# Performance work log

Hardware: AMD Instinct MI355X
Metric: run time of the kernel (lower is better)

## Reference

```python
import jax, jax.numpy as jnp
import numpy as np

B, T, F, H = 256, 128, 128, 512

def setup_inputs() -> dict:
    key = jax.random.key(0)
    ks = jax.random.split(key, 20)
    def xavier(k, shape):
        fan_in, fan_out = shape[1], shape[0]
        lim = np.sqrt(6.0 / (fan_in + fan_out)).astype(np.float32)
        return jax.random.uniform(k, shape, jnp.float32, -lim, lim)
    inp = {
        "x": jax.random.normal(ks[0], (B, T, F), jnp.float32),
        "m": (jax.random.uniform(ks[1], (B, T, F)) < 0.8).astype(jnp.float32),
        "d": jax.random.uniform(ks[2], (B, T, F), jnp.float32),
        "target_x": jax.random.normal(ks[3], (B, T, F), jnp.float32),
        "target_mask": (jax.random.uniform(ks[4], (B, T, F)) < 0.2).astype(jnp.float32),
        # TemporalDecay h: W [H,F], b [H]
        "td_h_W": xavier(ks[5], (H, F)), "td_h_b": jnp.zeros((H,), jnp.float32),
        # TemporalDecay x (diag): W [F,F], b [F]
        "td_x_W": xavier(ks[6], (F, F)), "td_x_b": jnp.zeros((F,), jnp.float32),
        # hist_reg Linear(H->F)
        "hist_W": xavier(ks[7], (F, H)), "hist_b": jnp.zeros((F,), jnp.float32),
        "feat_W": xavier(ks[8], (F, F)), "feat_b": jnp.zeros((F,), jnp.float32),
        # weight_combine Linear(2F->F)
        "wc_W": xavier(ks[9], (F, 2 * F)), "wc_b": jnp.zeros((F,), jnp.float32),
        # LSTMCell(2F -> H), PyTorch gate order i,f,g,o
        "W_ih": xavier(ks[10], (4 * H, 2 * F)), "W_hh": xavier(ks[11], (4 * H, H)),
        "b_ih": jnp.zeros((4 * H,), jnp.float32), "b_hh": jnp.zeros((4 * H,), jnp.float32),
    }
    return inp

def _rits_forward(x, m, d, target_x, target_mask,
                  td_h_W, td_h_b, td_x_W, td_x_b,
                  hist_W, hist_b, feat_W, feat_b, wc_W, wc_b,
                  W_ih, W_hh, b_ih, b_hh):
    Bx, Tx, Fx = x.shape
    Hx = td_h_W.shape[0]
    feat_mask = (1.0 - jnp.eye(Fx, dtype=x.dtype))
    feat_Wm_T = (feat_W * feat_mask).T              # [F,F]
    td_x_diag = jnp.diagonal(td_x_W)                # diag mask reduces matmul to elementwise

    def step(carry, inp):
        h, c, loss = carry
        x_t, m_t, d_t, tgt_t, ev_t = inp
        gamma_h = jnp.exp(-jax.nn.relu(d_t @ td_h_W.T + td_h_b))    # [B,H]
        gamma_x = jnp.exp(-jax.nn.relu(d_t * td_x_diag + td_x_b))   # [B,F]
        h = h * gamma_h
        x_hist = h @ hist_W.T + hist_b                              # [B,F]
        x_c = m_t * x_t + (1.0 - m_t) * x_hist
        z_h = x_c @ feat_Wm_T + feat_b
        alpha = jax.nn.sigmoid(jnp.concatenate([gamma_x, m_t], axis=1) @ wc_W.T + wc_b)
        c_h = alpha * z_h + (1.0 - alpha) * x_hist
        c_c = m_t * x_t + (1.0 - m_t) * c_h
        inputs = jnp.concatenate([c_c, m_t], axis=1)                # [B,2F]
        gates = inputs @ W_ih.T + b_ih + h @ W_hh.T + b_hh          # [B,4H]
        i_g, f_g, g_g, o_g = jnp.split(gates, 4, axis=1)
        c = jax.nn.sigmoid(f_g) * c + jax.nn.sigmoid(i_g) * jnp.tanh(g_g)
        h = jax.nn.sigmoid(o_g) * jnp.tanh(c)
        denom = ev_t.sum() + 1e-8
        loss = loss + (((x_hist - tgt_t) ** 2 * ev_t).sum()
                       + ((z_h - tgt_t) ** 2 * ev_t).sum()
                       + ((c_h - tgt_t) ** 2 * ev_t).sum()) / denom
        return (h, c, loss), c_c

    h0 = jnp.zeros((Bx, Hx), x.dtype)
    c0 = jnp.zeros((Bx, Hx), x.dtype)
    tm = lambda a: jnp.swapaxes(a, 0, 1)  # time-major [T,B,F]
    (_, _, loss), imps = jax.lax.scan(
        step, (h0, c0, jnp.float32(0.0)),
        (tm(x), tm(m), tm(d), tm(target_x), tm(target_mask)))
    imputations = jnp.swapaxes(imps, 0, 1)  # [B,T,F]
    return imputations, loss / max(Tx, 1)

def reference(x, m, d, target_x, target_mask,
              td_h_W, td_h_b, td_x_W, td_x_b,
              hist_W, hist_b, feat_W, feat_b, wc_W, wc_b,
              W_ih, W_hh, b_ih, b_hh):
    return _rits_forward(x, m, d, target_x, target_mask,
                         td_h_W, td_h_b, td_x_W, td_x_b,
                         hist_W, hist_b, feat_W, feat_b, wc_W, wc_b,
                         W_ih, W_hh, b_ih, b_hh)
```

## Files before the change

kernel.cpp:

```cpp
#include <hip/hip_runtime.h>

#define DEVINL __device__ __forceinline__

namespace {
constexpr int B = 256, T = 128, F = 128, H = 512;
constexpr int NBLK = 256;
constexpr int NTHR = 1024;

constexpr size_t OFF_NUM    = 0;
constexpr size_t OFF_DEN    = 128;
constexpr size_t OFF_WQCC   = 256;
constexpr size_t OFF_WQH    = OFF_WQCC + 64 * 2048;
constexpr size_t OFF_FSCC   = OFF_WQH + 128 * 2048;
constexpr size_t OFF_FSCHG  = OFF_FSCC + 2048;
constexpr size_t OFF_HISTQ  = OFF_FSCHG + 2048;
constexpr size_t OFF_FSCH   = OFF_HISTQ + 128 * 128;
constexpr size_t OFF_TD2    = OFF_FSCH + 128;
constexpr size_t OFF_FEAT2  = OFF_TD2 + 64 * 512;
constexpr size_t OFF_WC2    = OFF_FEAT2 + 64 * 128;
constexpr size_t OFF_BSUM   = OFF_WC2 + 128 * 128;
constexpr size_t OFF_FDIAG  = OFF_BSUM + 2048;
constexpr size_t WS_WORDS   = OFF_FDIAG + 128;

constexpr float ACT_S  = 15.875f;
constexpr float DEQ_CC = 1.f / (127.f * 15.875f);
constexpr float DEQ_H  = 1.f / (127.f * 127.f);
}

typedef _Float16 h2_t __attribute__((ext_vector_type(2)));

DEVINL h2_t as_h2(unsigned u) { union { unsigned u; h2_t h; } c; c.u = u; return c.h; }
DEVINL unsigned pack2(float a, float b) {
  union { h2_t h; unsigned u; } c;
  c.h = h2_t{(_Float16)a, (_Float16)b};
  return c.u;
}

#if defined(__has_builtin)
#if __has_builtin(__builtin_amdgcn_fdot2)
#define HAVE_FDOT2 1
#endif
#if __has_builtin(__builtin_amdgcn_sdot4)
#define HAVE_SDOT4 1
#endif
#endif
#ifdef HAVE_FDOT2
DEVINL float fdot2(h2_t a, h2_t b, float c) { return __builtin_amdgcn_fdot2(a, b, c, false); }
#else
DEVINL float fdot2(h2_t a, h2_t b, float c) {
  return fmaf((float)a.x, (float)b.x, fmaf((float)a.y, (float)b.y, c));
}
#endif
#ifdef HAVE_SDOT4
DEVINL int sdot4(int a, int b, int c) { return __builtin_amdgcn_sdot4(a, b, c, false); }
#else
DEVINL int sdot4(int a, int b, int c) {
  return c + ((a << 24) >> 24) * ((b << 24) >> 24)
           + ((a << 16) >> 24) * ((b << 16) >> 24)
           + ((a << 8) >> 24) * ((b << 8) >> 24)
           + (a >> 24) * (b >> 24);
}
#endif

DEVINL float fast_sig(float x)  { return 1.f / (1.f + __expf(-x)); }
DEVINL float fast_tanh(float x) { return 1.f - 2.f / (1.f + __expf(2.f * x)); }

DEVINL float wave_sum(float v) {
#pragma unroll
  for (int s = 32; s; s >>= 1) v += __shfl_down(v, s, 64);
  return v;
}
DEVINL float wave_max(float v) {
#pragma unroll
  for (int s = 32; s; s >>= 1) v = fmaxf(v, __shfl_down(v, s, 64));
  return v;
}

__global__ void prep_f16(const float* __restrict__ td_h_W, const float* __restrict__ feat_W,
                         const float* __restrict__ wc_W, const float* __restrict__ b_ih,
                         const float* __restrict__ b_hh,
                         unsigned* __restrict__ wsu, float* __restrict__ wsf) {
  int idx = blockIdx.x * blockDim.x + threadIdx.x;
  if (idx < 32768) {
    const int k2 = idx >> 9, j = idx & 511;
    wsu[OFF_TD2 + idx] = pack2(td_h_W[j * 128 + 2 * k2], td_h_W[j * 128 + 2 * k2 + 1]);
  } else if (idx < 40960) {
    const int i = idx - 32768, k2 = i >> 7, f = i & 127;
    wsu[OFF_FEAT2 + i] = pack2(feat_W[f * 128 + 2 * k2], feat_W[f * 128 + 2 * k2 + 1]);
  } else if (idx < 57344) {
    const int i = idx - 40960, k2 = i >> 7, f = i & 127;
    wsu[OFF_WC2 + i] = pack2(wc_W[f * 256 + 2 * k2], wc_W[f * 256 + 2 * k2 + 1]);
  } else if (idx < 59392) {
    const int i = idx - 57344, unit = i >> 2, g = i & 3;
    wsf[OFF_BSUM + i] = b_ih[g * 512 + unit] + b_hh[g * 512 + unit];
  } else if (idx < 59520) {
    const int f = idx - 59392;
    wsf[OFF_FDIAG + f] = (float)(_Float16)feat_W[f * 129];
  }
}

__global__ void prep_quant_wih(const float* __restrict__ Wih,
                               unsigned* __restrict__ wq, float* __restrict__ fscc) {
  const int col = blockIdx.x;
  const int unit = col >> 2, g = col & 3;
  const float* src = Wih + (size_t)(g * 512 + unit) * 256;
  const int t = threadIdx.x;
  const float4 v = ((const float4*)src)[t];
  float mx = fmaxf(fmaxf(fabsf(v.x), fabsf(v.y)), fmaxf(fabsf(v.z), fabsf(v.w)));
  mx = wave_max(mx);
  mx = __shfl(mx, 0, 64);
  const float s = (mx > 0.f) ? 127.f / mx : 0.f;
  const int q0 = __float2int_rn(v.x * s), q1 = __float2int_rn(v.y * s);
  const int q2 = __float2int_rn(v.z * s), q3 = __float2int_rn(v.w * s);
  wq[t * 2048 + col] =
      (q0 & 0xFF) | ((q1 & 0xFF) << 8) | ((q2 & 0xFF) << 16) | ((q3 & 0xFF) << 24);
  if (t == 0) fscc[col] = mx * DEQ_CC;
}

__global__ void prep_quant_whh(const float* __restrict__ Whh,
                               unsigned* __restrict__ wq, float* __restrict__ fschg) {
  const int col = blockIdx.x;
  const int unit = col >> 2, g = col & 3;
  const float* src = Whh + (size_t)(g * 512 + unit) * 512;
  const int t = threadIdx.x;
  const float4 v = ((const float4*)src)[t];
  float mx = fmaxf(fmaxf(fabsf(v.x), fabsf(v.y)), fmaxf(fabsf(v.z), fabsf(v.w)));
  mx = wave_max(mx);
  __shared__ float wm[2];
  if ((t & 63) == 0) wm[t >> 6] = mx;
  __syncthreads();
  const float maxv = fmaxf(wm[0], wm[1]);
  const float s = (maxv > 0.f) ? 127.f / maxv : 0.f;
  const int q0 = __float2int_rn(v.x * s), q1 = __float2int_rn(v.y * s);
  const int q2 = __float2int_rn(v.z * s), q3 = __float2int_rn(v.w * s);
  wq[t * 2048 + col] =
      (q0 & 0xFF) | ((q1 & 0xFF) << 8) | ((q2 & 0xFF) << 16) | ((q3 & 0xFF) << 24);
  if (t == 0) fschg[col] = maxv * DEQ_H;
}

__global__ void prep_quant_hist(const float* __restrict__ histW,
                                unsigned* __restrict__ histq, float* __restrict__ fsch) {
  const int f = blockIdx.x;
  const float* src = histW + (size_t)f * 512;
  const int t = threadIdx.x;
  const float4 v = ((const float4*)src)[t];
  float mx = fmaxf(fmaxf(fabsf(v.x), fabsf(v.y)), fmaxf(fabsf(v.z), fabsf(v.w)));
  mx = wave_max(mx);
  __shared__ float wm[2];
  if ((t & 63) == 0) wm[t >> 6] = mx;
  __syncthreads();
  const float maxv = fmaxf(wm[0], wm[1]);
  const float s = (maxv > 0.f) ? 127.f / maxv : 0.f;
  const int q0 = __float2int_rn(v.x * s), q1 = __float2int_rn(v.y * s);
  const int q2 = __float2int_rn(v.z * s), q3 = __float2int_rn(v.w * s);
  histq[t * 128 + f] =
      (q0 & 0xFF) | ((q1 & 0xFF) << 8) | ((q2 & 0xFF) << 16) | ((q3 & 0xFF) << 24);
  if (t == 0) fsch[f] = maxv * DEQ_H;
}

__global__ void __launch_bounds__(1024) rits_batch(
    const float* __restrict__ x, const float* __restrict__ m, const float* __restrict__ d,
    const float* __restrict__ tx, const float* __restrict__ tmask,
    const float* __restrict__ td_h_b, const float* __restrict__ td_x_W,
    const float* __restrict__ td_x_b, const float* __restrict__ hist_b,
    const float* __restrict__ feat_b, const float* __restrict__ wc_b,
    const unsigned* __restrict__ wsu, const float* __restrict__ wsf,
    float* __restrict__ num, float* __restrict__ den, float* __restrict__ out)
{
  const int tid = threadIdx.x;
  const int row = blockIdx.x;
  const int unit = tid & 511;
  const int kh = tid >> 9;

  __shared__ unsigned actq[64];
  __shared__ int hq[128];
  __shared__ unsigned d2[64];
  __shared__ unsigned xc2[64];
  __shared__ unsigned gxm2[128];
  __shared__ float xrow[128], mrow[128], drow[128], txrow[128], evrow[128];
  __shared__ int   partI[1024];
  __shared__ float partZ[1024], partA[1024];
  __shared__ int4  partHc[512], partHh[512];
  __shared__ float redA[2], redB[2];

  const float4 bs    = *(const float4*)(wsf + OFF_BSUM + 4 * unit);
  const float4 fscc4 = *(const float4*)(wsf + OFF_FSCC + 4 * unit);
  const float4 fsch4 = *(const float4*)(wsf + OFF_FSCHG + 4 * unit);
  const float tdb = td_h_b[unit];
  const int fc = tid & 127;
  const float hb = hist_b[fc], fb = feat_b[fc], wb = wc_b[fc];
  const float fd = wsf[OFF_FDIAG + fc];
  const float dxw = td_x_W[fc * 129], dxb = td_x_b[fc];
  const float fsch_f = wsf[OFF_FSCH + fc];

  float h0 = 0.f, c0 = 0.f;

  for (int t = 0; t < T; ++t) {
    const int base = (row * T + t) * F;
    float xh_r = 0.f, xc_r = 0.f;

    if (tid < 640) {
      const int a = tid >> 7, f = tid & 127;
      const float v = (a == 0 ? x[base + f] : a == 1 ? m[base + f] : a == 2 ? d[base + f]
                       : a == 3 ? tx[base + f] : tmask[base + f]);
      if      (a == 0) xrow[f]  = v;
      else if (a == 1) mrow[f]  = v;
      else if (a == 2) drow[f]  = v;
      else if (a == 3) txrow[f] = v;
      else             evrow[f] = v;
    } else if (tid < 704) {
      const int k2 = tid - 640;
      d2[k2] = pack2(d[base + 2 * k2], d[base + 2 * k2 + 1]);
    } else if (tid < 768) {
      const int q = tid - 704;
      gxm2[64 + q] = pack2(m[base + 2 * q], m[base + 2 * q + 1]);
    } else if (tid < 800) {
      const int w = tid - 768;
      const int b4 = base + 4 * w;
      const int q0 = __float2int_rn(m[b4] * ACT_S);
      const int q1 = __float2int_rn(m[b4 + 1] * ACT_S);
      const int q2 = __float2int_rn(m[b4 + 2] * ACT_S);
      const int q3 = __float2int_rn(m[b4 + 3] * ACT_S);
      actq[32 + w] =
          (q0 & 0xFF) | ((q1 & 0xFF) << 8) | ((q2 & 0xFF) << 16) | ((q3 & 0xFF) << 24);
    }
    __syncthreads();

    if (tid < 512) {
      float g0 = tdb;
#pragma unroll 8
      for (int k2 = 0; k2 < 64; ++k2)
        g0 = fdot2(as_h2(wsu[OFF_TD2 + (k2 << 9) + tid]), as_h2(d2[k2]), g0);
      h0 *= __expf(-fmaxf(g0, 0.f));
      int q = __float2int_rn(h0 * 127.f);
      const int a1 = __shfl_down(q, 1, 64), a2 = __shfl_down(q, 2, 64), a3 = __shfl_down(q, 3, 64);
      if ((tid & 3) == 0)
        hq[tid >> 2] =
            (q & 0xFF) | ((a1 & 0xFF) << 8) | ((a2 & 0xFF) << 16) | ((a3 & 0xFF) << 24);
    }
    __syncthreads();

    {
      const int kq = tid >> 7;
      int isum = 0;
#pragma unroll 8
      for (int k = 0; k < 16; ++k) {
        const int k4 = kq * 16 + k;
        isum = sdot4((int)wsu[OFF_HISTQ + (k4 << 7) + fc], hq[k4], isum);
      }
      partI[tid] = isum;
    }
    __syncthreads();

    if (tid < 128) {
      int isum = 0;
#pragma unroll
      for (int i = 0; i < 8; ++i) isum += partI[tid + 128 * i];
      xh_r = fmaf((float)isum, fsch_f, hb);
      const float gx = __expf(-fmaxf(fmaf(drow[tid], dxw, dxb), 0.f));
      const float mv = mrow[tid];
      xc_r = mv * xrow[tid] + (1.f - mv) * xh_r;
      const float xcs = __shfl_down(xc_r, 1, 64);
      const float gxs = __shfl_down(gx, 1, 64);
      if (!(tid & 1)) {
        xc2[tid >> 1]  = pack2(xc_r, xcs);
        gxm2[tid >> 1] = pack2(gx, gxs);
      }
    }
    __syncthreads();

    {
      const int kq = tid >> 7;
      float zs = 0.f;
#pragma unroll 8
      for (int k = 0; k < 8; ++k) {
        const int k2 = kq * 8 + k;
        zs = fdot2(as_h2(wsu[OFF_FEAT2 + (k2 << 7) + fc]), as_h2(xc2[k2]), zs);
      }
      partZ[tid] = zs;
      float as = 0.f;
#pragma unroll 8
      for (int k = 0; k < 16; ++k) {
        const int k2 = kq * 16 + k;
        as = fdot2(as_h2(wsu[OFF_WC2 + (k2 << 7) + fc]), as_h2(gxm2[k2]), as);
      }
      partA[tid] = as;
    }
    __syncthreads();

    if (tid < 128) {
      float z = fb, aa = wb;
#pragma unroll
      for (int i = 0; i < 8; ++i) { z += partZ[tid + 128 * i]; aa += partA[tid + 128 * i]; }
      z -= xc_r * fd;
      const float al = fast_sig(aa);
      const float ch = al * z + (1.f - al) * xh_r;
      const float mv = mrow[tid];
      const float cc = mv * xrow[tid] + (1.f - mv) * ch;
      out[base + tid] = cc;
      const float ev = evrow[tid], tg = txrow[tid];
      const float e1 = xh_r - tg, e2 = z - tg, e3 = ch - tg;
      const float s1 = wave_sum(ev * (e1 * e1 + e2 * e2 + e3 * e3));
      const float s2 = wave_sum(ev);
      if ((tid & 63) == 0) { redA[tid >> 6] = s1; redB[tid >> 6] = s2; }
      int qc = __float2int_rn(fminf(fmaxf(cc, -8.f), 8.f) * ACT_S);
      const int c1s = __shfl_down(qc, 1, 64), c2s = __shfl_down(qc, 2, 64), c3s = __shfl_down(qc, 3, 64);
      if (!(tid & 3))
        actq[tid >> 2] =
            (qc & 0xFF) | ((c1s & 0xFF) << 8) | ((c2s & 0xFF) << 16) | ((c3s & 0xFF) << 24);
    }
    __syncthreads();

    {
      if (tid == 1023) {
        atomicAdd(&num[t], redA[0] + redA[1]);
        atomicAdd(&den[t], redB[0] + redB[1]);
      }
      int ci = 0, cf = 0, cg = 0, co = 0;
      const unsigned* wq = wsu + OFF_WQCC + 4 * unit;
#pragma unroll 8
      for (int k = 0; k < 32; ++k) {
        const int k4 = kh * 32 + k;
        const uint4 w = *(const uint4*)(wq + (k4 << 11));
        const int a0 = (int)actq[k4];
        ci = sdot4((int)w.x, a0, ci); cf = sdot4((int)w.y, a0, cf);
        cg = sdot4((int)w.z, a0, cg); co = sdot4((int)w.w, a0, co);
      }
      int hi = 0, hf = 0, hg = 0, ho = 0;
      const unsigned* wh = wsu + OFF_WQH + 4 * unit;
#pragma unroll 8
      for (int k = 0; k < 64; ++k) {
        const int k4 = kh * 64 + k;
        const uint4 w = *(const uint4*)(wh + (k4 << 11));
        const int a0 = hq[k4];
        hi = sdot4((int)w.x, a0, hi); hf = sdot4((int)w.y, a0, hf);
        hg = sdot4((int)w.z, a0, hg); ho = sdot4((int)w.w, a0, ho);
      }
      if (tid >= 512) {
        partHc[unit] = int4{ci, cf, cg, co};
        partHh[unit] = int4{hi, hf, hg, ho};
      }
      __syncthreads();
      if (tid < 512) {
        const int4 pc = partHc[unit], ph = partHh[unit];
        const float ai = bs.x + fscc4.x * (float)(ci + pc.x) + fsch4.x * (float)(hi + ph.x);
        const float af = bs.y + fscc4.y * (float)(cf + pc.y) + fsch4.y * (float)(hf + ph.y);
        const float ag = bs.z + fscc4.z * (float)(cg + pc.z) + fsch4.z * (float)(hg + ph.z);
        const float ao = bs.w + fscc4.w * (float)(co + pc.w) + fsch4.w * (float)(ho + ph.w);
        const float ig = fast_sig(ai), fg = fast_sig(af);
        const float gg = fast_tanh(ag), og = fast_sig(ao);
        c0 = fg * c0 + ig * gg;
        h0 = og * fast_tanh(c0);
      }
    }
    __syncthreads();
  }
}

__global__ void finalize(const float* __restrict__ num, const float* __restrict__ den,
                         float* __restrict__ out) {
  __shared__ float red[2];
  const int t = threadIdx.x;
  float v = num[t] / (den[t] + 1e-8f);
  v = wave_sum(v);
  if ((t & 63) == 0) red[t >> 6] = v;
  __syncthreads();
  if (t == 0) out[(size_t)B * T * F] = (red[0] + red[1]) / (float)T;
}

extern "C" void kernel_launch(void* const* d_in, const int* in_sizes, int n_in,
                              void* d_out, int out_size, void* d_ws, size_t ws_size,
                              hipStream_t stream) {
  const float* x      = (const float*)d_in[0];
  const float* m      = (const float*)d_in[1];
  const float* d      = (const float*)d_in[2];
  const float* tx     = (const float*)d_in[3];
  const float* tmask  = (const float*)d_in[4];
  const float* td_h_W = (const float*)d_in[5];
  const float* td_h_b = (const float*)d_in[6];
  const float* td_x_W = (const float*)d_in[7];
  const float* td_x_b = (const float*)d_in[8];
  const float* hist_W = (const float*)d_in[9];
  const float* hist_b = (const float*)d_in[10];
  const float* feat_W = (const float*)d_in[11];
  const float* feat_b = (const float*)d_in[12];
  const float* wc_W   = (const float*)d_in[13];
  const float* wc_b   = (const float*)d_in[14];
  const float* W_ih   = (const float*)d_in[15];
  const float* W_hh   = (const float*)d_in[16];
  const float* b_ih   = (const float*)d_in[17];
  const float* b_hh   = (const float*)d_in[18];

  float*    wsf = (float*)d_ws;
  unsigned* wsu = (unsigned*)d_ws;
  float*    out = (float*)d_out;

  if (ws_size < WS_WORDS * 4) return;

  hipMemsetAsync(d_ws, 0, 256 * sizeof(float), stream);
  prep_f16<<<dim3((59520 + 255) / 256), dim3(256), 0, stream>>>(
      td_h_W, feat_W, wc_W, b_ih, b_hh, wsu, wsf);
  prep_quant_wih<<<dim3(2048), dim3(64), 0, stream>>>(
      W_ih, wsu + OFF_WQCC, wsf + OFF_FSCC);
  prep_quant_whh<<<dim3(2048), dim3(128), 0, stream>>>(
      W_hh, wsu + OFF_WQH, wsf + OFF_FSCHG);
  prep_quant_hist<<<dim3(128), dim3(128), 0, stream>>>(
      hist_W, wsu + OFF_HISTQ, wsf + OFF_FSCH);
  rits_batch<<<dim3(NBLK), dim3(NTHR), 0, stream>>>(
      x, m, d, tx, tmask, td_h_b, td_x_W, td_x_b, hist_b, feat_b, wc_b,
      wsu, wsf, wsf + OFF_NUM, wsf + OFF_DEN, out);
  finalize<<<dim3(1), dim3(128), 0, stream>>>(wsf + OFF_NUM, wsf + OFF_DEN, out);
}
```

Measured before the change: 2.436 ms.

## Warp-specialize RITS step with LDS flag sync and overlapped LSTM matvecs

Replaces the per-step chain of block-wide __syncthreads with warp specialization. Two waves handle the feature path (hist regression, feature regression, combine, loss, next-step decay prefetch). The other 14 waves run the LSTM int8 matvecs and signal each other through LDS atomic flags with spin-waits. The h-part of the LSTM gate matvec now starts as soon as hq is ready and overlaps the feature-side work, and next-step inputs and decay are computed ahead with double-buffered shared arrays. Weight layouts are transposed so each feature thread streams its own contiguous row with uint4 loads. The cost is spin-wait polling, a guard-limited spin that could break silently, and only 128 threads doing the feature path serially.

```diff
diff --git a/kernel.cpp b/kernel.cpp
--- a/kernel.cpp
+++ b/kernel.cpp
@@ -25,6 +25,8 @@
 constexpr float ACT_S  = 15.875f;
 constexpr float DEQ_CC = 1.f / (127.f * 15.875f);
 constexpr float DEQ_H  = 1.f / (127.f * 127.f);
+
+constexpr int FH = 0, FX = 1, FD = 2, FA = 3, FS = 4, FL = 5;
 }
 
 typedef _Float16 h2_t __attribute__((ext_vector_type(2)));
@@ -34,6 +36,9 @@
   union { h2_t h; unsigned u; } c;
   c.h = h2_t{(_Float16)a, (_Float16)b};
   return c.u;
+}
+DEVINL unsigned pack4i(int a, int b, int c, int d) {
+  return (a & 0xFF) | ((b & 0xFF) << 8) | ((c & 0xFF) << 16) | ((d & 0xFF) << 24);
 }
 
 #if defined(__has_builtin)
@@ -76,19 +81,30 @@
   return v;
 }
 
+DEVINL void flag_add(unsigned* p) {
+  __hip_atomic_fetch_add(p, 1u, __ATOMIC_RELEASE, __HIP_MEMORY_SCOPE_WORKGROUP);
+}
+DEVINL void spin_ge(const unsigned* p, unsigned tgt) {
+  int guard = 0;
+  while (__hip_atomic_load(p, __ATOMIC_ACQUIRE, __HIP_MEMORY_SCOPE_WORKGROUP) < tgt) {
+    __builtin_amdgcn_s_sleep(1);
+    if (++guard > (1 << 24)) break;
+  }
+}
+
 __global__ void prep_f16(const float* __restrict__ td_h_W, const float* __restrict__ feat_W,
                          const float* __restrict__ wc_W, const float* __restrict__ b_ih,
                          const float* __restrict__ b_hh,
                          unsigned* __restrict__ wsu, float* __restrict__ wsf) {
   int idx = blockIdx.x * blockDim.x + threadIdx.x;
   if (idx < 32768) {
-    const int k2 = idx >> 9, j = idx & 511;
-    wsu[OFF_TD2 + idx] = pack2(td_h_W[j * 128 + 2 * k2], td_h_W[j * 128 + 2 * k2 + 1]);
+    const int u = idx >> 6, k2 = idx & 63;
+    wsu[OFF_TD2 + idx] = pack2(td_h_W[u * 128 + 2 * k2], td_h_W[u * 128 + 2 * k2 + 1]);
   } else if (idx < 40960) {
-    const int i = idx - 32768, k2 = i >> 7, f = i & 127;
+    const int i = idx - 32768, f = i >> 6, k2 = i & 63;
     wsu[OFF_FEAT2 + i] = pack2(feat_W[f * 128 + 2 * k2], feat_W[f * 128 + 2 * k2 + 1]);
   } else if (idx < 57344) {
-    const int i = idx - 40960, k2 = i >> 7, f = i & 127;
+    const int i = idx - 40960, f = i >> 7, k2 = i & 127;
     wsu[OFF_WC2 + i] = pack2(wc_W[f * 256 + 2 * k2], wc_W[f * 256 + 2 * k2 + 1]);
   } else if (idx < 59392) {
     const int i = idx - 57344, unit = i >> 2, g = i & 3;
@@ -110,10 +126,8 @@
   mx = wave_max(mx);
   mx = __shfl(mx, 0, 64);
   const float s = (mx > 0.f) ? 127.f / mx : 0.f;
-  const int q0 = __float2int_rn(v.x * s), q1 = __float2int_rn(v.y * s);
-  const int q2 = __float2int_rn(v.z * s), q3 = __float2int_rn(v.w * s);
-  wq[t * 2048 + col] =
-      (q0 & 0xFF) | ((q1 & 0xFF) << 8) | ((q2 & 0xFF) << 16) | ((q3 & 0xFF) << 24);
+  wq[t * 2048 + col] = pack4i(__float2int_rn(v.x * s), __float2int_rn(v.y * s),
+                              __float2int_rn(v.z * s), __float2int_rn(v.w * s));
   if (t == 0) fscc[col] = mx * DEQ_CC;
 }
 
@@ -131,10 +145,8 @@
   __syncthreads();
   const float maxv = fmaxf(wm[0], wm[1]);
   const float s = (maxv > 0.f) ? 127.f / maxv : 0.f;
-  const int q0 = __float2int_rn(v.x * s), q1 = __float2int_rn(v.y * s);
-  const int q2 = __float2int_rn(v.z * s), q3 = __float2int_rn(v.w * s);
-  wq[t * 2048 + col] =
-      (q0 & 0xFF) | ((q1 & 0xFF) << 8) | ((q2 & 0xFF) << 16) | ((q3 & 0xFF) << 24);
+  wq[t * 2048 + col] = pack4i(__float2int_rn(v.x * s), __float2int_rn(v.y * s),
+                              __float2int_rn(v.z * s), __float2int_rn(v.w * s));
   if (t == 0) fschg[col] = maxv * DEQ_H;
 }
 
@@ -151,14 +163,12 @@
   __syncthreads();
   const float maxv = fmaxf(wm[0], wm[1]);
   const float s = (maxv > 0.f) ? 127.f / maxv : 0.f;
-  const int q0 = __float2int_rn(v.x * s), q1 = __float2int_rn(v.y * s);
-  const int q2 = __float2int_rn(v.z * s), q3 = __float2int_rn(v.w * s);
-  histq[t * 128 + f] =
-      (q0 & 0xFF) | ((q1 & 0xFF) << 8) | ((q2 & 0xFF) << 16) | ((q3 & 0xFF) << 24);
+  histq[f * 128 + t] = pack4i(__float2int_rn(v.x * s), __float2int_rn(v.y * s),
+                              __float2int_rn(v.z * s), __float2int_rn(v.w * s));
   if (t == 0) fsch[f] = maxv * DEQ_H;
 }
 
-__global__ void __launch_bounds__(1024) rits_batch(
+__global__ void __launch_bounds__(NTHR) rits_batch(
     const float* __restrict__ x, const float* __restrict__ m, const float* __restrict__ d,
     const float* __restrict__ tx, const float* __restrict__ tmask,
     const float* __restrict__ td_h_b, const float* __restrict__ td_x_W,
@@ -169,191 +179,240 @@
 {
   const int tid = threadIdx.x;
   const int row = blockIdx.x;
-  const int unit = tid & 511;
-  const int kh = tid >> 9;
-
-  __shared__ unsigned actq[64];
-  __shared__ int hq[128];
-  __shared__ unsigned d2[64];
-  __shared__ unsigned xc2[64];
-  __shared__ unsigned gxm2[128];
-  __shared__ float xrow[128], mrow[128], drow[128], txrow[128], evrow[128];
-  __shared__ int   partI[1024];
-  __shared__ float partZ[1024], partA[1024];
-  __shared__ int4  partHc[512], partHh[512];
-  __shared__ float redA[2], redB[2];
-
-  const float4 bs    = *(const float4*)(wsf + OFF_BSUM + 4 * unit);
-  const float4 fscc4 = *(const float4*)(wsf + OFF_FSCC + 4 * unit);
-  const float4 fsch4 = *(const float4*)(wsf + OFF_FSCHG + 4 * unit);
-  const float tdb = td_h_b[unit];
-  const int fc = tid & 127;
-  const float hb = hist_b[fc], fb = feat_b[fc], wb = wc_b[fc];
-  const float fd = wsf[OFF_FDIAG + fc];
-  const float dxw = td_x_W[fc * 129], dxb = td_x_b[fc];
-  const float fsch_f = wsf[OFF_FSCH + fc];
-
-  float h0 = 0.f, c0 = 0.f;
-
-  for (int t = 0; t < T; ++t) {
-    const int base = (row * T + t) * F;
-    float xh_r = 0.f, xc_r = 0.f;
-
-    if (tid < 640) {
-      const int a = tid >> 7, f = tid & 127;
-      const float v = (a == 0 ? x[base + f] : a == 1 ? m[base + f] : a == 2 ? d[base + f]
-                       : a == 3 ? tx[base + f] : tmask[base + f]);
-      if      (a == 0) xrow[f]  = v;
-      else if (a == 1) mrow[f]  = v;
-      else if (a == 2) drow[f]  = v;
-      else if (a == 3) txrow[f] = v;
-      else             evrow[f] = v;
-    } else if (tid < 704) {
-      const int k2 = tid - 640;
-      d2[k2] = pack2(d[base + 2 * k2], d[base + 2 * k2 + 1]);
-    } else if (tid < 768) {
-      const int q = tid - 704;
-      gxm2[64 + q] = pack2(m[base + 2 * q], m[base + 2 * q + 1]);
-    } else if (tid < 800) {
-      const int w = tid - 768;
-      const int b4 = base + 4 * w;
-      const int q0 = __float2int_rn(m[b4] * ACT_S);
-      const int q1 = __float2int_rn(m[b4 + 1] * ACT_S);
-      const int q2 = __float2int_rn(m[b4 + 2] * ACT_S);
-      const int q3 = __float2int_rn(m[b4 + 3] * ACT_S);
-      actq[32 + w] =
-          (q0 & 0xFF) | ((q1 & 0xFF) << 8) | ((q2 & 0xFF) << 16) | ((q3 & 0xFF) << 24);
+
+  __shared__ __align__(16) unsigned hq_s[128];
+  __shared__ __align__(16) unsigned actq_s[2][64];
+  __shared__ __align__(16) unsigned gxm2_s[2][128];
+  __shared__ __align__(16) unsigned d2_s[64];
+  __shared__ __align__(16) unsigned xc2_s[64];
+  __shared__ __align__(16) float gexp_s[512];
+  __shared__ __align__(16) float h_s[512];
+  __shared__ __align__(16) int4 partH_s[4][512];
+  __shared__ __align__(16) int4 partC_s[2][512];
+  __shared__ unsigned flg[6];
+
+  if (tid < 512) { h_s[tid] = 0.f; gexp_s[tid] = 0.f; }
+  if (tid < 6) flg[tid] = 0u;
+  __syncthreads();
+
+  if (tid < 128) {
+    const int f = tid;
+    const float hb = hist_b[f], fb = feat_b[f], wb = wc_b[f];
+    const float fd = wsf[OFF_FDIAG + f], fsf = wsf[OFF_FSCH + f];
+    const float dxw = td_x_W[f * 129], dxb = td_x_b[f];
+    const float4 tdb4 = *(const float4*)(td_h_b + 4 * tid);
+
+    float x_r, m_r, d_r, tx_r, ev_r;
+    {
+      const size_t b0 = (size_t)row * T * F + f;
+      x_r = x[b0]; m_r = m[b0]; d_r = d[b0]; tx_r = tx[b0]; ev_r = tmask[b0];
+      const float gx = __expf(-fmaxf(fmaf(d_r, dxw, dxb), 0.f));
+      const float gxs = __shfl_down(gx, 1, 64);
+      const float ms  = __shfl_down(m_r, 1, 64);
+      if (!(f & 1)) {
+        gxm2_s[0][f >> 1] = pack2(gx, gxs);
+        gxm2_s[0][64 + (f >> 1)] = pack2(m_r, ms);
+      }
+      const int qm = __float2int_rn(m_r * ACT_S);
+      const int q1 = __shfl_down(qm, 1, 64), q2 = __shfl_down(qm, 2, 64), q3 = __shfl_down(qm, 3, 64);
+      if (!(f & 3)) actq_s[0][32 + (f >> 2)] = pack4i(qm, q1, q2, q3);
     }
-    __syncthreads();
-
-    if (tid < 512) {
-      float g0 = tdb;
+
+    for (int t = 0; t < T; ++t) {
+      const size_t base = ((size_t)row * T + t) * F;
+      const int par = t & 1;
+
+      if (t) { spin_ge(&flg[FL], 8u * (unsigned)t); __threadfence_block(); }
+      {
+        const float4 h4 = *(const float4*)(h_s + 4 * tid);
+        const float4 g4 = *(const float4*)(gexp_s + 4 * tid);
+        hq_s[tid] = pack4i(__float2int_rn(h4.x * g4.x * 127.f),
+                           __float2int_rn(h4.y * g4.y * 127.f),
+                           __float2int_rn(h4.z * g4.z * 127.f),
+                           __float2int_rn(h4.w * g4.w * 127.f));
+      }
+      __threadfence_block();
+      if (!(tid & 63)) flag_add(&flg[FH]);
+      spin_ge(&flg[FH], 2u * (unsigned)(t + 1)); __threadfence_block();
+
+      int is = 0;
+      {
+        const uint4* hw = (const uint4*)(wsu + OFF_HISTQ + (size_t)f * 128);
+        const uint4* hq4 = (const uint4*)hq_s;
 #pragma unroll 8
-      for (int k2 = 0; k2 < 64; ++k2)
-        g0 = fdot2(as_h2(wsu[OFF_TD2 + (k2 << 9) + tid]), as_h2(d2[k2]), g0);
-      h0 *= __expf(-fmaxf(g0, 0.f));
-      int q = __float2int_rn(h0 * 127.f);
-      const int a1 = __shfl_down(q, 1, 64), a2 = __shfl_down(q, 2, 64), a3 = __shfl_down(q, 3, 64);
-      if ((tid & 3) == 0)
-        hq[tid >> 2] =
-            (q & 0xFF) | ((a1 & 0xFF) << 8) | ((a2 & 0xFF) << 16) | ((a3 & 0xFF) << 24);
+        for (int k = 0; k < 32; ++k) {
+          const uint4 w = hw[k], a = hq4[k];
+          is = sdot4((int)w.x, (int)a.x, is);
+          is = sdot4((int)w.y, (int)a.y, is);
+          is = sdot4((int)w.z, (int)a.z, is);
+          is = sdot4((int)w.w, (int)a.w, is);
+        }
+      }
+      const float xh = fmaf((float)is, fsf, hb);
+      const float xc = m_r * x_r + (1.f - m_r) * xh;
+      {
+        const float xcs = __shfl_down(xc, 1, 64);
+        if (!(f & 1)) xc2_s[f >> 1] = pack2(xc, xcs);
+      }
+      __threadfence_block();
+      if (!(tid & 63)) flag_add(&flg[FX]);
+      spin_ge(&flg[FX], 2u * (unsigned)(t + 1)); __threadfence_block();
+
+      float z = fb, aa = wb;
+      {
+        const uint4* fw = (const uint4*)(wsu + OFF_FEAT2 + (size_t)f * 64);
+        const uint4* xw = (const uint4*)xc2_s;
+#pragma unroll 8
+        for (int k = 0; k < 16; ++k) {
+          const uint4 w = fw[k], v = xw[k];
+          z = fdot2(as_h2(w.x), as_h2(v.x), z);
+          z = fdot2(as_h2(w.y), as_h2(v.y), z);
+          z = fdot2(as_h2(w.z), as_h2(v.z), z);
+          z = fdot2(as_h2(w.w), as_h2(v.w), z);
+        }
+        const uint4* ww = (const uint4*)(wsu + OFF_WC2 + (size_t)f * 128);
+        const uint4* gw = (const uint4*)gxm2_s[par];
+#pragma unroll 8
+        for (int k = 0; k < 32; ++k) {
+          const uint4 w = ww[k], g = gw[k];
+          aa = fdot2(as_h2(w.x), as_h2(g.x), aa);
+          aa = fdot2(as_h2(w.y), as_h2(g.y), aa);
+          aa = fdot2(as_h2(w.z), as_h2(g.z), aa);
+          aa = fdot2(as_h2(w.w), as_h2(g.w), aa);
+        }
+      }
+      z -= xc * fd;
+      const float al = fast_sig(aa);
+      const float ch = al * z + (1.f - al) * xh;
+      const float cc = m_r * x_r + (1.f - m_r) * ch;
+      out[base + f] = cc;
+      const float e1 = xh - tx_r, e2 = z - tx_r, e3 = ch - tx_r;
+      const float s1 = wave_sum(ev_r * (e1 * e1 + e2 * e2 + e3 * e3));
+      const float s2 = wave_sum(ev_r);
+      if (!(tid & 63)) { atomicAdd(&num[t], s1); atomicAdd(&den[t], s2); }
+
+      {
+        const int qc = __float2int_rn(fminf(fmaxf(cc, -8.f), 8.f) * ACT_S);
+        const int c1 = __shfl_down(qc, 1, 64), c2 = __shfl_down(qc, 2, 64), c3 = __shfl_down(qc, 3, 64);
+        if (!(f & 3)) actq_s[par][f >> 2] = pack4i(qc, c1, c2, c3);
+      }
+      __threadfence_block();
+      if (!(tid & 63)) flag_add(&flg[FA]);
+
+      if (t + 1 < T) {
+        const size_t b2 = base + F + f;
+        x_r = x[b2]; m_r = m[b2]; d_r = d[b2]; tx_r = tx[b2]; ev_r = tmask[b2];
+        const float gx = __expf(-fmaxf(fmaf(d_r, dxw, dxb), 0.f));
+        const float gxs = __shfl_down(gx, 1, 64);
+        const float ms  = __shfl_down(m_r, 1, 64);
+        const float dsh = __shfl_down(d_r, 1, 64);
+        if (!(f & 1)) {
+          gxm2_s[par ^ 1][f >> 1] = pack2(gx, gxs);
+          gxm2_s[par ^ 1][64 + (f >> 1)] = pack2(m_r, ms);
+          d2_s[f >> 1] = pack2(d_r, dsh);
+        }
+        const int qm = __float2int_rn(m_r * ACT_S);
+        const int q1 = __shfl_down(qm, 1, 64), q2 = __shfl_down(qm, 2, 64), q3 = __shfl_down(qm, 3, 64);
+        if (!(f & 3)) actq_s[par ^ 1][32 + (f >> 2)] = pack4i(qm, q1, q2, q3);
+        __threadfence_block();
+        if (!(tid & 63)) flag_add(&flg[FD]);
+        spin_ge(&flg[FD], 2u * (unsigned)(t + 1)); __threadfence_block();
+        float g0 = tdb4.x, g1 = tdb4.y, g2 = tdb4.z, g3 = tdb4.w;
+        const uint4* t0 = (const uint4*)(wsu + OFF_TD2 + ((size_t)tid * 4) * 64);
+        const uint4* dw = (const uint4*)d2_s;
+#pragma unroll 4
+        for (int k = 0; k < 16; ++k) {
+          const uint4 dd = dw[k];
+          uint4 w = t0[k];
+          g0 = fdot2(as_h2(w.x), as_h2(dd.x), g0); g0 = fdot2(as_h2(w.y), as_h2(dd.y), g0);
+          g0 = fdot2(as_h2(w.z), as_h2(dd.z), g0); g0 = fdot2(as_h2(w.w), as_h2(dd.w), g0);
+          w = t0[k + 16];
+          g1 = fdot2(as_h2(w.x), as_h2(dd.x), g1); g1 = fdot2(as_h2(w.y), as_h2(dd.y), g1);
+          g1 = fdot2(as_h2(w.z), as_h2(dd.z), g1); g1 = fdot2(as_h2(w.w), as_h2(dd.w), g1);
+          w = t0[k + 32];
+          g2 = fdot2(as_h2(w.x), as_h2(dd.x), g2); g2 = fdot2(as_h2(w.y), as_h2(dd.y), g2);
+          g2 = fdot2(as_h2(w.z), as_h2(dd.z), g2); g2 = fdot2(as_h2(w.w), as_h2(dd.w), g2);
+          w = t0[k + 48];
+          g3 = fdot2(as_h2(w.x), as_h2(dd.x), g3); g3 = fdot2(as_h2(w.y), as_h2(dd.y), g3);
+          g3 = fdot2(as_h2(w.z), as_h2(dd.z), g3); g3 = fdot2(as_h2(w.w), as_h2(dd.w), g3);
+        }
+        *(float4*)(gexp_s + 4 * tid) = float4{
+            __expf(-fmaxf(g0, 0.f)), __expf(-fmaxf(g1, 0.f)),
+            __expf(-fmaxf(g2, 0.f)), __expf(-fmaxf(g3, 0.f))};
+      }
     }
-    __syncthreads();
-
-    {
-      const int kq = tid >> 7;
-      int isum = 0;
+  } else {
+    const int st = tid - 128;
+    float4 bs{}, fscc4{}, fsch4{};
+    float c0 = 0.f;
+    if (st < 512) {
+      bs    = *(const float4*)(wsf + OFF_BSUM  + 4 * st);
+      fscc4 = *(const float4*)(wsf + OFF_FSCC  + 4 * st);
+      fsch4 = *(const float4*)(wsf + OFF_FSCHG + 4 * st);
+    }
+    for (int t = 0; t < T; ++t) {
+      const int par = t & 1;
+      const unsigned tg = (unsigned)(t + 1);
+      spin_ge(&flg[FH], 2u * tg); __threadfence_block();
+#pragma unroll 1
+      for (int it = 0; it < 4; ++it) {
+        const int j = st + 896 * it;
+        if (j >= 3072) break;
+        if (j < 2048) {
+          const int unit = j & 511, kq = j >> 9;
+          const uint4* wp = (const uint4*)(wsu + OFF_WQH) + (size_t)(kq * 32) * 512 + unit;
+          const unsigned* aw = hq_s + kq * 32;
+          int4 acc{0, 0, 0, 0};
 #pragma unroll 8
-      for (int k = 0; k < 16; ++k) {
-        const int k4 = kq * 16 + k;
-        isum = sdot4((int)wsu[OFF_HISTQ + (k4 << 7) + fc], hq[k4], isum);
-      }
-      partI[tid] = isum;
-    }
-    __syncthreads();
-
-    if (tid < 128) {
-      int isum = 0;
-#pragma unroll
-      for (int i = 0; i < 8; ++i) isum += partI[tid + 128 * i];
-      xh_r = fmaf((float)isum, fsch_f, hb);
-      const float gx = __expf(-fmaxf(fmaf(drow[tid], dxw, dxb), 0.f));
-      const float mv = mrow[tid];
-      xc_r = mv * xrow[tid] + (1.f - mv) * xh_r;
-      const float xcs = __shfl_down(xc_r, 1, 64);
-      const float gxs = __shfl_down(gx, 1, 64);
-      if (!(tid & 1)) {
-        xc2[tid >> 1]  = pack2(xc_r, xcs);
-        gxm2[tid >> 1] = pack2(gx, gxs);
-      }
-    }
-    __syncthreads();
-
-    {
-      const int kq = tid >> 7;
-      float zs = 0.f;
+          for (int k = 0; k < 32; ++k) {
+            const uint4 w = wp[(size_t)k * 512];
+            const int a0 = (int)aw[k];
+            acc.x = sdot4((int)w.x, a0, acc.x);
+            acc.y = sdot4((int)w.y, a0, acc.y);
+            acc.z = sdot4((int)w.z, a0, acc.z);
+            acc.w = sdot4((int)w.w, a0, acc.w);
+          }
+          partH_s[kq][unit] = acc;
+        } else {
+          const int jj = j - 2048;
+          const int unit = jj & 511;
+          const int kh = 1 - (jj >> 9);
+          if (kh == 0) { spin_ge(&flg[FA], 2u * tg); __threadfence_block(); }
+          const uint4* wp = (const uint4*)(wsu + OFF_WQCC) + (size_t)(kh * 32) * 512 + unit;
+          const unsigned* aw = actq_s[par] + kh * 32;
+          int4 acc{0, 0, 0, 0};
 #pragma unroll 8
-      for (int k = 0; k < 8; ++k) {
-        const int k2 = kq * 8 + k;
-        zs = fdot2(as_h2(wsu[OFF_FEAT2 + (k2 << 7) + fc]), as_h2(xc2[k2]), zs);
-      }
-      partZ[tid] = zs;
-      float as = 0.f;
-#pragma unroll 8
-      for (int k = 0; k < 16; ++k) {
-        const int k2 = kq * 16 + k;
-        as = fdot2(as_h2(wsu[OFF_WC2 + (k2 << 7) + fc]), as_h2(gxm2[k2]), as);
-      }
-      partA[tid] = as;
-    }
-    __syncthreads();
-
-    if (tid < 128) {
-      float z = fb, aa = wb;
-#pragma unroll
-      for (int i = 0; i < 8; ++i) { z += partZ[tid + 128 * i]; aa += partA[tid + 128 * i]; }
-      z -= xc_r * fd;
-      const float al = fast_sig(aa);
-      const float ch = al * z + (1.f - al) * xh_r;
-      const float mv = mrow[tid];
-      const float cc = mv * xrow[tid] + (1.f - mv) * ch;
-      out[base + tid] = cc;
-      const float ev = evrow[tid], tg = txrow[tid];
-      const float e1 = xh_r - tg, e2 = z - tg, e3 = ch - tg;
-      const float s1 = wave_sum(ev * (e1 * e1 + e2 * e2 + e3 * e3));
-      const float s2 = wave_sum(ev);
-      if ((tid & 63) == 0) { redA[tid >> 6] = s1; redB[tid >> 6] = s2; }
-      int qc = __float2int_rn(fminf(fmaxf(cc, -8.f), 8.f) * ACT_S);
-      const int c1s = __shfl_down(qc, 1, 64), c2s = __shfl_down(qc, 2, 64), c3s = __shfl_down(qc, 3, 64);
-      if (!(tid & 3))
-        actq[tid >> 2] =
-            (qc & 0xFF) | ((c1s & 0xFF) << 8) | ((c2s & 0xFF) << 16) | ((c3s & 0xFF) << 24);
-    }
-    __syncthreads();
-
-    {
-      if (tid == 1023) {
-        atomicAdd(&num[t], redA[0] + redA[1]);
-        atomicAdd(&den[t], redB[0] + redB[1]);
-      }
-      int ci = 0, cf = 0, cg = 0, co = 0;
-      const unsigned* wq = wsu + OFF_WQCC + 4 * unit;
-#pragma unroll 8
-      for (int k = 0; k < 32; ++k) {
-        const int k4 = kh * 32 + k;
-        const uint4 w = *(const uint4*)(wq + (k4 << 11));
-        const int a0 = (int)actq[k4];
-        ci = sdot4((int)w.x, a0, ci); cf = sdot4((int)w.y, a0, cf);
-        cg = sdot4((int)w.z, a0, cg); co = sdot4((int)w.w, a0, co);
-      }
-      int hi = 0, hf = 0, hg = 0, ho = 0;
-      const unsigned* wh = wsu + OFF_WQH + 4 * unit;
-#pragma unroll 8
-      for (int k = 0; k < 64; ++k) {
-        const int k4 = kh * 64 + k;
-        const uint4 w = *(const uint4*)(wh + (k4 << 11));
-        const int a0 = hq[k4];
-        hi = sdot4((int)w.x, a0, hi); hf = sdot4((int)w.y, a0, hf);
-        hg = sdot4((int)w.z, a0, hg); ho = sdot4((int)w.w, a0, ho);
-      }
-      if (tid >= 512) {
-        partHc[unit] = int4{ci, cf, cg, co};
-        partHh[unit] = int4{hi, hf, hg, ho};
-      }
-      __syncthreads();
-      if (tid < 512) {
-        const int4 pc = partHc[unit], ph = partHh[unit];
-        const float ai = bs.x + fscc4.x * (float)(ci + pc.x) + fsch4.x * (float)(hi + ph.x);
-        const float af = bs.y + fscc4.y * (float)(cf + pc.y) + fsch4.y * (float)(hf + ph.y);
-        const float ag = bs.z + fscc4.z * (float)(cg + pc.z) + fsch4.z * (float)(hg + ph.z);
-        const float ao = bs.w + fscc4.w * (float)(co + pc.w) + fsch4.w * (float)(ho + ph.w);
+          for (int k = 0; k < 32; ++k) {
+            const uint4 w = wp[(size_t)k * 512];
+            const int a0 = (int)aw[k];
+            acc.x = sdot4((int)w.x, a0, acc.x);
+            acc.y = sdot4((int)w.y, a0, acc.y);
+            acc.z = sdot4((int)w.z, a0, acc.z);
+            acc.w = sdot4((int)w.w, a0, acc.w);
+          }
+          partC_s[kh][unit] = acc;
+        }
+      }
+      __threadfence_block();
+      if (!(tid & 63)) flag_add(&flg[FS]);
+      spin_ge(&flg[FS], 14u * tg); __threadfence_block();
+
+      if (st < 512) {
+        const int4 p0 = partH_s[0][st], p1 = partH_s[1][st],
+                   p2 = partH_s[2][st], p3 = partH_s[3][st];
+        const int4 q0 = partC_s[0][st], q1 = partC_s[1][st];
+        const float ai = bs.x + fscc4.x * (float)(q0.x + q1.x) + fsch4.x * (float)(p0.x + p1.x + p2.x + p3.x);
+        const float af = bs.y + fscc4.y * (float)(q0.y + q1.y) + fsch4.y * (float)(p0.y + p1.y + p2.y + p3.y);
+        const float ag = bs.z + fscc4.z * (float)(q0.z + q1.z) + fsch4.z * (float)(p0.z + p1.z + p2.z + p3.z);
+        const float ao = bs.w + fscc4.w * (float)(q0.w + q1.w) + fsch4.w * (float)(p0.w + p1.w + p2.w + p3.w);
         const float ig = fast_sig(ai), fg = fast_sig(af);
         const float gg = fast_tanh(ag), og = fast_sig(ao);
         c0 = fg * c0 + ig * gg;
-        h0 = og * fast_tanh(c0);
+        h_s[st] = og * fast_tanh(c0);
+        __threadfence_block();
+        if (!(tid & 63)) flag_add(&flg[FL]);
       }
     }
-    __syncthreads();
   }
 }
 
```

Result: slower. 3.037 ms (+24.7%).

## Fold next-step temporal decay into LSTM phase and drop a per-step barrier

Applied to the files above, without the earlier changes.

The decay of the hidden state for step t+1 is now computed by the upper half-block, which was idle during the LSTM gate epilogue. It uses a double-buffered, prefetched copy of the next d row and a per-unit contiguous fp16 layout for td_h_W that allows 16-byte loads. The hidden state is decayed and quantized right after the LSTM update, which removes a whole phase and one __syncthreads per timestep. The last step skips the gate computation. The risk is extra shared memory and more work for the upper-half threads, which lengthens the critical path of that phase.

```diff
diff --git a/kernel.cpp b/kernel.cpp
--- a/kernel.cpp
+++ b/kernel.cpp
@@ -35,6 +35,9 @@
   c.h = h2_t{(_Float16)a, (_Float16)b};
   return c.u;
 }
+DEVINL unsigned pack4i(int a, int b, int c, int d) {
+  return (a & 0xFF) | ((b & 0xFF) << 8) | ((c & 0xFF) << 16) | ((d & 0xFF) << 24);
+}
 
 #if defined(__has_builtin)
 #if __has_builtin(__builtin_amdgcn_fdot2)
@@ -82,8 +85,8 @@
                          unsigned* __restrict__ wsu, float* __restrict__ wsf) {
   int idx = blockIdx.x * blockDim.x + threadIdx.x;
   if (idx < 32768) {
-    const int k2 = idx >> 9, j = idx & 511;
-    wsu[OFF_TD2 + idx] = pack2(td_h_W[j * 128 + 2 * k2], td_h_W[j * 128 + 2 * k2 + 1]);
+    const int u = idx >> 6, k2 = idx & 63;
+    wsu[OFF_TD2 + idx] = pack2(td_h_W[u * 128 + 2 * k2], td_h_W[u * 128 + 2 * k2 + 1]);
   } else if (idx < 40960) {
     const int i = idx - 32768, k2 = i >> 7, f = i & 127;
     wsu[OFF_FEAT2 + i] = pack2(feat_W[f * 128 + 2 * k2], feat_W[f * 128 + 2 * k2 + 1]);
@@ -110,10 +113,8 @@
   mx = wave_max(mx);
   mx = __shfl(mx, 0, 64);
   const float s = (mx > 0.f) ? 127.f / mx : 0.f;
-  const int q0 = __float2int_rn(v.x * s), q1 = __float2int_rn(v.y * s);
-  const int q2 = __float2int_rn(v.z * s), q3 = __float2int_rn(v.w * s);
-  wq[t * 2048 + col] =
-      (q0 & 0xFF) | ((q1 & 0xFF) << 8) | ((q2 & 0xFF) << 16) | ((q3 & 0xFF) << 24);
+  wq[t * 2048 + col] = pack4i(__float2int_rn(v.x * s), __float2int_rn(v.y * s),
+                              __float2int_rn(v.z * s), __float2int_rn(v.w * s));
   if (t == 0) fscc[col] = mx * DEQ_CC;
 }
 
@@ -131,10 +132,8 @@
   __syncthreads();
   const float maxv = fmaxf(wm[0], wm[1]);
   const float s = (maxv > 0.f) ? 127.f / maxv : 0.f;
-  const int q0 = __float2int_rn(v.x * s), q1 = __float2int_rn(v.y * s);
-  const int q2 = __float2int_rn(v.z * s), q3 = __float2int_rn(v.w * s);
-  wq[t * 2048 + col] =
-      (q0 & 0xFF) | ((q1 & 0xFF) << 8) | ((q2 & 0xFF) << 16) | ((q3 & 0xFF) << 24);
+  wq[t * 2048 + col] = pack4i(__float2int_rn(v.x * s), __float2int_rn(v.y * s),
+                              __float2int_rn(v.z * s), __float2int_rn(v.w * s));
   if (t == 0) fschg[col] = maxv * DEQ_H;
 }
 
@@ -151,10 +150,8 @@
   __syncthreads();
   const float maxv = fmaxf(wm[0], wm[1]);
   const float s = (maxv > 0.f) ? 127.f / maxv : 0.f;
-  const int q0 = __float2int_rn(v.x * s), q1 = __float2int_rn(v.y * s);
-  const int q2 = __float2int_rn(v.z * s), q3 = __float2int_rn(v.w * s);
-  histq[t * 128 + f] =
-      (q0 & 0xFF) | ((q1 & 0xFF) << 8) | ((q2 & 0xFF) << 16) | ((q3 & 0xFF) << 24);
+  histq[t * 128 + f] = pack4i(__float2int_rn(v.x * s), __float2int_rn(v.y * s),
+                              __float2int_rn(v.z * s), __float2int_rn(v.w * s));
   if (t == 0) fsch[f] = maxv * DEQ_H;
 }
 
@@ -172,15 +169,16 @@
   const int unit = tid & 511;
   const int kh = tid >> 9;
 
-  __shared__ unsigned actq[64];
-  __shared__ int hq[128];
-  __shared__ unsigned d2[64];
-  __shared__ unsigned xc2[64];
-  __shared__ unsigned gxm2[128];
+  __shared__ __align__(16) unsigned actq[64];
+  __shared__ __align__(16) int hq[128];
+  __shared__ __align__(16) unsigned d2b[128];
+  __shared__ __align__(16) unsigned xc2[64];
+  __shared__ __align__(16) unsigned gxm2[128];
   __shared__ float xrow[128], mrow[128], drow[128], txrow[128], evrow[128];
   __shared__ int   partI[1024];
   __shared__ float partZ[1024], partA[1024];
-  __shared__ int4  partHc[512], partHh[512];
+  __shared__ __align__(16) int4 partHc[512], partHh[512];
+  __shared__ float gexp_s[512];
   __shared__ float redA[2], redB[2];
 
   const float4 bs    = *(const float4*)(wsf + OFF_BSUM + 4 * unit);
@@ -194,6 +192,7 @@
   const float fsch_f = wsf[OFF_FSCH + fc];
 
   float h0 = 0.f, c0 = 0.f;
+  if (tid < 128) hq[tid] = 0;
 
   for (int t = 0; t < T; ++t) {
     const int base = (row * T + t) * F;
@@ -209,34 +208,18 @@
       else if (a == 3) txrow[f] = v;
       else             evrow[f] = v;
     } else if (tid < 704) {
-      const int k2 = tid - 640;
-      d2[k2] = pack2(d[base + 2 * k2], d[base + 2 * k2 + 1]);
+      if (t < T - 1) {
+        const int k2 = tid - 640;
+        d2b[((t + 1) & 1) * 64 + k2] = pack2(d[base + F + 2 * k2], d[base + F + 2 * k2 + 1]);
+      }
     } else if (tid < 768) {
       const int q = tid - 704;
       gxm2[64 + q] = pack2(m[base + 2 * q], m[base + 2 * q + 1]);
     } else if (tid < 800) {
       const int w = tid - 768;
       const int b4 = base + 4 * w;
-      const int q0 = __float2int_rn(m[b4] * ACT_S);
-      const int q1 = __float2int_rn(m[b4 + 1] * ACT_S);
-      const int q2 = __float2int_rn(m[b4 + 2] * ACT_S);
-      const int q3 = __float2int_rn(m[b4 + 3] * ACT_S);
-      actq[32 + w] =
-          (q0 & 0xFF) | ((q1 & 0xFF) << 8) | ((q2 & 0xFF) << 16) | ((q3 & 0xFF) << 24);
-    }
-    __syncthreads();
-
-    if (tid < 512) {
-      float g0 = tdb;
-#pragma unroll 8
-      for (int k2 = 0; k2 < 64; ++k2)
-        g0 = fdot2(as_h2(wsu[OFF_TD2 + (k2 << 9) + tid]), as_h2(d2[k2]), g0);
-      h0 *= __expf(-fmaxf(g0, 0.f));
-      int q = __float2int_rn(h0 * 127.f);
-      const int a1 = __shfl_down(q, 1, 64), a2 = __shfl_down(q, 2, 64), a3 = __shfl_down(q, 3, 64);
-      if ((tid & 3) == 0)
-        hq[tid >> 2] =
-            (q & 0xFF) | ((a1 & 0xFF) << 8) | ((a2 & 0xFF) << 16) | ((a3 & 0xFF) << 24);
+      actq[32 + w] = pack4i(__float2int_rn(m[b4] * ACT_S), __float2int_rn(m[b4 + 1] * ACT_S),
+                            __float2int_rn(m[b4 + 2] * ACT_S), __float2int_rn(m[b4 + 3] * ACT_S));
     }
     __syncthreads();
 
@@ -305,17 +288,17 @@
       if ((tid & 63) == 0) { redA[tid >> 6] = s1; redB[tid >> 6] = s2; }
       int qc = __float2int_rn(fminf(fmaxf(cc, -8.f), 8.f) * ACT_S);
       const int c1s = __shfl_down(qc, 1, 64), c2s = __shfl_down(qc, 2, 64), c3s = __shfl_down(qc, 3, 64);
-      if (!(tid & 3))
-        actq[tid >> 2] =
-            (qc & 0xFF) | ((c1s & 0xFF) << 8) | ((c2s & 0xFF) << 16) | ((c3s & 0xFF) << 24);
-    }
-    __syncthreads();
+      if (!(tid & 3)) actq[tid >> 2] = pack4i(qc, c1s, c2s, c3s);
+    }
+    __syncthreads();
+
+    if (tid == 1023) {
+      atomicAdd(&num[t], redA[0] + redA[1]);
+      atomicAdd(&den[t], redB[0] + redB[1]);
+    }
+    if (t == T - 1) break;
 
     {
-      if (tid == 1023) {
-        atomicAdd(&num[t], redA[0] + redA[1]);
-        atomicAdd(&den[t], redB[0] + redB[1]);
-      }
       int ci = 0, cf = 0, cg = 0, co = 0;
       const unsigned* wq = wsu + OFF_WQCC + 4 * unit;
 #pragma unroll 8
@@ -339,6 +322,18 @@
       if (tid >= 512) {
         partHc[unit] = int4{ci, cf, cg, co};
         partHh[unit] = int4{hi, hf, hg, ho};
+        float g0 = tdb;
+        const uint4* tw = (const uint4*)(wsu + OFF_TD2 + (size_t)unit * 64);
+        const uint4* dw = (const uint4*)(d2b + ((t + 1) & 1) * 64);
+#pragma unroll 4
+        for (int q = 0; q < 16; ++q) {
+          const uint4 w = tw[q], dd = dw[q];
+          g0 = fdot2(as_h2(w.x), as_h2(dd.x), g0);
+          g0 = fdot2(as_h2(w.y), as_h2(dd.y), g0);
+          g0 = fdot2(as_h2(w.z), as_h2(dd.z), g0);
+          g0 = fdot2(as_h2(w.w), as_h2(dd.w), g0);
+        }
+        gexp_s[unit] = __expf(-fmaxf(g0, 0.f));
       }
       __syncthreads();
       if (tid < 512) {
@@ -351,6 +346,10 @@
         const float gg = fast_tanh(ag), og = fast_sig(ao);
         c0 = fg * c0 + ig * gg;
         h0 = og * fast_tanh(c0);
+        const float hv = h0 * gexp_s[unit];
+        int q = __float2int_rn(hv * 127.f);
+        const int a1 = __shfl_down(q, 1, 64), a2 = __shfl_down(q, 2, 64), a3 = __shfl_down(q, 3, 64);
+        if (!(tid & 3)) hq[tid >> 2] = pack4i(q, a1, a2, a3);
       }
     }
     __syncthreads();
```

Measured after the change: 3.248 ms. 33.3% more time.
